# Performance work log

Hardware: AMD Instinct MI355X
Metric: run time of the kernel (lower is better)

The kernel has to match this reference:

```python
import jax, jax.numpy as jnp
import numpy as np

B, S, D = 64, 2048, 64

def setup_inputs() -> dict:
    key = jax.random.key(0)
    k1, k2, k3, k4 = jax.random.split(key, 4)
    query = jax.random.normal(k1, (B, S, D), dtype=jnp.float32)
    keyt = jax.random.normal(k2, (B, S, D), dtype=jnp.float32)
    value = jax.random.normal(k3, (B, S, D), dtype=jnp.float32)
    mask = jax.random.randint(k4, (1, S, S), 0, 2, dtype=jnp.int32)
    return {"query": query, "key": keyt, "value": value, "mask": mask}

def reference(query, key, value, mask):
    # scores: [B, S, S]
    scale = jnp.sqrt(jnp.asarray(value.shape[-1], dtype=query.dtype))
    scores = jnp.einsum('bqd,bkd->bqk', query, key) / scale
    scores = jnp.where(mask == 0, jnp.asarray(-1e9, dtype=scores.dtype), scores)
    attention_weights = jax.nn.softmax(scores, axis=-1)
    # dropout p=0.0 -> identity
    context = jnp.einsum('bqk,bkd->bqd', attention_weights, value)
    return (context, attention_weights)
```

## Files before the change

kernel.cpp:

```cpp
#include <hip/hip_runtime.h>

#define NB 64
#define NS 2048
#define ND 64
#define KSTEP 64
#define NIT (NS / KSTEP)

typedef __bf16 bf16x8 __attribute__((ext_vector_type(8)));
typedef float f32x4 __attribute__((ext_vector_type(4)));
typedef unsigned int u32;
typedef u32 u32x2 __attribute__((ext_vector_type(2)));
typedef u32 u32x4 __attribute__((ext_vector_type(4)));
typedef unsigned short u16;
typedef u16 u16x8 __attribute__((ext_vector_type(8)));

#define C2F 0.18033688011112042f

__device__ __forceinline__ float fexp2(float x) {
#if __has_builtin(__builtin_amdgcn_exp2f)
  return __builtin_amdgcn_exp2f(x);
#else
  return exp2f(x);
#endif
}
__device__ __forceinline__ float flog2(float x) {
#if __has_builtin(__builtin_amdgcn_logf)
  return __builtin_amdgcn_logf(x);
#else
  return log2f(x);
#endif
}

#define TILE_BARRIER()                                   \
  do {                                                   \
    asm volatile("s_waitcnt lgkmcnt(0)" ::: "memory");   \
    __builtin_amdgcn_s_barrier();                        \
    asm volatile("" ::: "memory");                       \
  } while (0)

__device__ __forceinline__ u16 f2bs(float x) {
  __bf16 h = (__bf16)x;
  return __builtin_bit_cast(u16, h);
}

__device__ __forceinline__ bf16x8 cvt8(f32x4 a, f32x4 b) {
  bf16x8 r;
  r[0] = (__bf16)a[0]; r[1] = (__bf16)a[1]; r[2] = (__bf16)a[2]; r[3] = (__bf16)a[3];
  r[4] = (__bf16)b[0]; r[5] = (__bf16)b[1]; r[6] = (__bf16)b[2]; r[7] = (__bf16)b[3];
  return r;
}

__global__ __launch_bounds__(256) void prep_cast_k(const float* __restrict__ K,
                                                   u16* __restrict__ Kbf) {
  const size_t i = ((size_t)blockIdx.x * 256 + threadIdx.x) * 8;
  f32x4 a = __builtin_nontemporal_load((const f32x4*)(K + i));
  f32x4 b = __builtin_nontemporal_load((const f32x4*)(K + i + 4));
  *(bf16x8*)(Kbf + i) = cvt8(a, b);
}

__global__ __launch_bounds__(256) void prep_transp_v(const float* __restrict__ V,
                                                     u16* __restrict__ VT) {
  __shared__ __attribute__((aligned(16))) u16 T[64][72];
  const int b = blockIdx.x >> 5, kt = blockIdx.x & 31;
  const float* src = V + ((size_t)b * NS + kt * 64) * ND;
  {
    const int k = threadIdx.x >> 2, d0 = (threadIdx.x & 3) * 16;
    const float* p = src + (size_t)k * ND + d0;
    f32x4 a0 = __builtin_nontemporal_load((const f32x4*)p);
    f32x4 a1 = __builtin_nontemporal_load((const f32x4*)(p + 4));
    f32x4 a2 = __builtin_nontemporal_load((const f32x4*)(p + 8));
    f32x4 a3 = __builtin_nontemporal_load((const f32x4*)(p + 12));
    *(bf16x8*)&T[k][d0]     = cvt8(a0, a1);
    *(bf16x8*)&T[k][d0 + 8] = cvt8(a2, a3);
  }
  __syncthreads();
  const int d = threadIdx.x >> 2, k0 = (threadIdx.x & 3) * 16;
  u16x8 r0, r1;
#pragma unroll
  for (int j = 0; j < 8; ++j) {
    const int P0 = k0 + j, P1 = k0 + 8 + j;
    const int s0 = 32 * (P0 >> 5) + 16 * ((P0 >> 2) & 1) + 4 * ((P0 >> 3) & 3) + (P0 & 3);
    const int s1 = 32 * (P1 >> 5) + 16 * ((P1 >> 2) & 1) + 4 * ((P1 >> 3) & 3) + (P1 & 3);
    r0[j] = T[s0][d];
    r1[j] = T[s1][d];
  }
  u16* dst = VT + ((size_t)b * ND + d) * NS + kt * 64 + k0;
  *(u16x8*)dst = r0;
  *(u16x8*)(dst + 8) = r1;
}

__global__ __launch_bounds__(256) void prep_pack_mask(const int* __restrict__ M,
                                                      unsigned long long* __restrict__ Mb) {
  const size_t i = (size_t)blockIdx.x * 256 + threadIdx.x;
  const unsigned long long bal = __ballot(M[i] != 0);
  if ((threadIdx.x & 63) == 0) Mb[i >> 6] = bal;
}

template <bool PRE>
__global__ __launch_bounds__(512, 3) void DotProductAttention_22436909154804_kernel(
    const float* __restrict__ Q, const float* __restrict__ K,
    const float* __restrict__ V, const int* __restrict__ M,
    const u16* __restrict__ Kbf, const u16* __restrict__ VTbf,
    const u32* __restrict__ Mb, float* __restrict__ ctx, float* __restrict__ wts) {
  __shared__ __attribute__((aligned(16))) u16 Kt[2][64][72];
  __shared__ __attribute__((aligned(16))) u16 Vt[2][64][72];
  __shared__ float Rs[2][64];

  const int tid  = threadIdx.x;
  const int lane = tid & 63;
  const int w    = tid >> 6;
  const int wq   = w & 3;
  const int kt   = w >> 2;
  const int g    = lane >> 4;
  const int c    = lane & 15;

  const int bid = blockIdx.x;
  const int vb  = (bid & 7) * 256 + (bid >> 3);
  const int b   = vb >> 5;
  const int qt  = vb & 31;
  const int q0w = qt * 64 + wq * 16;
  const size_t bq = (size_t)b * NS;

  const float* qp = Q + (bq + q0w + c) * ND + 8 * g;
  f32x4 qa = __builtin_nontemporal_load((const f32x4*)qp);
  f32x4 qb = __builtin_nontemporal_load((const f32x4*)(qp + 4));
  const bf16x8 qf0 = cvt8(qa, qb);
  qa = __builtin_nontemporal_load((const f32x4*)(qp + 32));
  qb = __builtin_nontemporal_load((const f32x4*)(qp + 36));
  const bf16x8 qf1 = cvt8(qa, qb);

  const u16* Kbb = PRE ? (Kbf + bq * ND) : (const u16*)nullptr;
  const u16* VTb = PRE ? (VTbf + bq * ND) : (const u16*)nullptr;
  const float* Kb32 = K + bq * ND;
  const float* Vb32 = V + bq * ND;
  const int* Mr  = M + (size_t)(q0w + c) * NS + kt * 32;
  const u32* Mbr = Mb + (size_t)(q0w + c) * (NS / 32) + kt;

  const bool isK = tid < 256;
  const int st   = tid & 255;

  auto msel = [](float e, u32 mm, int idx) -> float {
    u32 keep = (u32)(((int)(mm << (31 - idx))) >> 31);
    return __uint_as_float(__float_as_uint(e) & keep);
  };

  u16x8 sp0, sp1;
  f32x4 kf0, kf1, kf2, kf3;
  auto issueK1 = [&](int kb) {
    if (PRE) {
      const int r = tid >> 3, cc = (tid & 7) * 8;
      sp0 = *(const u16x8*)(Kbb + (size_t)(kb + r) * ND + cc);
    } else if (isK) {
      const int r = st >> 2, cc = (st & 3) * 16;
      const float* p = Kb32 + (size_t)(kb + r) * ND + cc;
      kf0 = *(const f32x4*)p;       kf1 = *(const f32x4*)(p + 4);
      kf2 = *(const f32x4*)(p + 8); kf3 = *(const f32x4*)(p + 12);
    }
  };
  auto writeK1 = [&](int buf) {
    if (PRE) {
      const int r = tid >> 3, cc = (tid & 7) * 8;
      *(u16x8*)&Kt[buf][r][cc] = sp0;
    } else if (isK) {
      const int r = st >> 2, cc = (st & 3) * 16;
      *(bf16x8*)&Kt[buf][r][cc]     = cvt8(kf0, kf1);
      *(bf16x8*)&Kt[buf][r][cc + 8] = cvt8(kf2, kf3);
    }
  };
  auto issueKV = [&](int kb) {
    if (PRE) {
      if (isK) {
        const int r = st >> 2, cc = (st & 3) * 16;
        const u16* p = Kbb + (size_t)(kb + r) * ND + cc;
        sp0 = *(const u16x8*)p; sp1 = *(const u16x8*)(p + 8);
      } else {
        const int d = st >> 2, kc = (st & 3) * 16;
        const u16* p = VTb + (size_t)d * NS + kb + kc;
        sp0 = *(const u16x8*)p; sp1 = *(const u16x8*)(p + 8);
      }
    } else {
      if (isK) {
        const int r = st >> 2, cc = (st & 3) * 16;
        const float* p = Kb32 + (size_t)(kb + r) * ND + cc;
        kf0 = *(const f32x4*)p;       kf1 = *(const f32x4*)(p + 4);
        kf2 = *(const f32x4*)(p + 8); kf3 = *(const f32x4*)(p + 12);
      } else {
        const int k = st >> 2, d0 = (st & 3) * 16;
        const float* p = Vb32 + (size_t)(kb + k) * ND + d0;
        kf0 = *(const f32x4*)p;       kf1 = *(const f32x4*)(p + 4);
        kf2 = *(const f32x4*)(p + 8); kf3 = *(const f32x4*)(p + 12);
      }
    }
  };
  auto writeKV = [&](int buf) {
    if (PRE) {
      if (isK) {
        const int r = st >> 2, cc = (st & 3) * 16;
        *(u16x8*)&Kt[buf][r][cc] = sp0; *(u16x8*)&Kt[buf][r][cc + 8] = sp1;
      } else {
        const int d = st >> 2, kc = (st & 3) * 16;
        *(u16x8*)&Vt[buf][d][kc] = sp0; *(u16x8*)&Vt[buf][d][kc + 8] = sp1;
      }
    } else {
      if (isK) {
        const int r = st >> 2, cc = (st & 3) * 16;
        *(bf16x8*)&Kt[buf][r][cc]     = cvt8(kf0, kf1);
        *(bf16x8*)&Kt[buf][r][cc + 8] = cvt8(kf2, kf3);
      } else {
        const int k = st >> 2, d0 = (st & 3) * 16;
        bf16x8 v0 = cvt8(kf0, kf1), v1 = cvt8(kf2, kf3);
#pragma unroll
        for (int j = 0; j < 8; ++j) {
          Vt[buf][d0 + j][k]     = __builtin_bit_cast(u16, v0[j]);
          Vt[buf][d0 + 8 + j][k] = __builtin_bit_cast(u16, v1[j]);
        }
      }
    }
  };

  const f32x4 zz = {0.f, 0.f, 0.f, 0.f};

  float rs = 0.f;
  issueK1(0);
  writeK1(0);
  __syncthreads();
  for (int it = 0; it < NIT; ++it) {
    const int cur = it & 1, kb = it * KSTEP;
    if (it + 1 < NIT) issueK1(kb + KSTEP);
    u32 mm = 0;
    if (PRE) mm = Mbr[kb >> 5];
#pragma unroll
    for (int j = 0; j < 2; ++j) {
      bf16x8 a0 = *(const bf16x8*)&Kt[cur][kt * 32 + 16 * j + c][8 * g];
      bf16x8 a1 = *(const bf16x8*)&Kt[cur][kt * 32 + 16 * j + c][32 + 8 * g];
      f32x4 s = __builtin_amdgcn_mfma_f32_16x16x32_bf16(a0, qf0, zz, 0, 0, 0);
      s = __builtin_amdgcn_mfma_f32_16x16x32_bf16(a1, qf1, s, 0, 0, 0);
      if (PRE) {
        rs += msel(fexp2(s[0] * C2F), mm, 16 * j + 4 * g + 0)
            + msel(fexp2(s[1] * C2F), mm, 16 * j + 4 * g + 1)
            + msel(fexp2(s[2] * C2F), mm, 16 * j + 4 * g + 2)
            + msel(fexp2(s[3] * C2F), mm, 16 * j + 4 * g + 3);
      } else {
        const int4 m4 = *(const int4*)(Mr + kb + 16 * j + 4 * g);
        rs += (m4.x ? fexp2(s[0] * C2F) : 0.f)
            + (m4.y ? fexp2(s[1] * C2F) : 0.f)
            + (m4.z ? fexp2(s[2] * C2F) : 0.f)
            + (m4.w ? fexp2(s[3] * C2F) : 0.f);
      }
    }
    if (it + 1 < NIT) writeK1((it + 1) & 1);
    TILE_BARRIER();
  }
  rs += __shfl_xor(rs, 16);
  rs += __shfl_xor(rs, 32);
  issueKV(0);
  if (lane < 16) Rs[kt][wq * 16 + c] = rs;
  __syncthreads();
  const float l2inv = -flog2(Rs[0][wq * 16 + c] + Rs[1][wq * 16 + c]);
  writeKV(0);
  __syncthreads();

  f32x4 acc[4] = {zz, zz, zz, zz};
  float* wrow = wts + (bq + q0w + c) * NS + kt * 32;
  for (int it = 0; it < NIT; ++it) {
    const int cur = it & 1, kb = it * KSTEP;
    if (it + 1 < NIT) issueKV(kb + KSTEP);
    u32 mm = 0;
    if (PRE) mm = Mbr[kb >> 5];

    u32 wpk[4];
#pragma unroll
    for (int j = 0; j < 2; ++j) {
      bf16x8 a0 = *(const bf16x8*)&Kt[cur][kt * 32 + 16 * j + c][8 * g];
      bf16x8 a1 = *(const bf16x8*)&Kt[cur][kt * 32 + 16 * j + c][32 + 8 * g];
      f32x4 s = __builtin_amdgcn_mfma_f32_16x16x32_bf16(a0, qf0, zz, 0, 0, 0);
      s = __builtin_amdgcn_mfma_f32_16x16x32_bf16(a1, qf1, s, 0, 0, 0);
      float w0, w1, w2, w3;
      if (PRE) {
        w0 = msel(fexp2(fmaf(s[0], C2F, l2inv)), mm, 16 * j + 4 * g + 0);
        w1 = msel(fexp2(fmaf(s[1], C2F, l2inv)), mm, 16 * j + 4 * g + 1);
        w2 = msel(fexp2(fmaf(s[2], C2F, l2inv)), mm, 16 * j + 4 * g + 2);
        w3 = msel(fexp2(fmaf(s[3], C2F, l2inv)), mm, 16 * j + 4 * g + 3);
      } else {
        const int4 m4 = *(const int4*)(Mr + kb + 16 * j + 4 * g);
        w0 = m4.x ? fexp2(fmaf(s[0], C2F, l2inv)) : 0.f;
        w1 = m4.y ? fexp2(fmaf(s[1], C2F, l2inv)) : 0.f;
        w2 = m4.z ? fexp2(fmaf(s[2], C2F, l2inv)) : 0.f;
        w3 = m4.w ? fexp2(fmaf(s[3], C2F, l2inv)) : 0.f;
      }
      f32x4 wv = {w0, w1, w2, w3};
      __builtin_nontemporal_store(wv, (f32x4*)(wrow + kb + 16 * j + 4 * g));
      wpk[2 * j]     = (u32)f2bs(w0) | ((u32)f2bs(w1) << 16);
      wpk[2 * j + 1] = (u32)f2bs(w2) | ((u32)f2bs(w3) << 16);
    }

    u32x4 wu = {wpk[0], wpk[1], wpk[2], wpk[3]};
    bf16x8 wb = __builtin_bit_cast(bf16x8, wu);
#pragma unroll
    for (int dt = 0; dt < 4; ++dt) {
      bf16x8 va;
      if (PRE) {
        va = *(const bf16x8*)&Vt[cur][dt * 16 + c][kt * 32 + 8 * g];
      } else {
        u32x2 vlo = *(const u32x2*)&Vt[cur][dt * 16 + c][kt * 32 + 4 * g];
        u32x2 vhi = *(const u32x2*)&Vt[cur][dt * 16 + c][kt * 32 + 16 + 4 * g];
        u32x4 vau = {vlo.x, vlo.y, vhi.x, vhi.y};
        va = __builtin_bit_cast(bf16x8, vau);
      }
      acc[dt] = __builtin_amdgcn_mfma_f32_16x16x32_bf16(va, wb, acc[dt], 0, 0, 0);
    }

    if (it + 1 < NIT) writeKV((it + 1) & 1);
    TILE_BARRIER();
  }

  float* red = (float*)&Kt[0][0][0] + wq * 1088;
  if (kt == 1) {
#pragma unroll
    for (int dt = 0; dt < 4; ++dt)
      *(f32x4*)&red[c * 68 + dt * 16 + 4 * g] = acc[dt];
  }
  __syncthreads();
  if (kt == 0) {
    float* crow = ctx + (bq + q0w + c) * ND;
#pragma unroll
    for (int dt = 0; dt < 4; ++dt) {
      f32x4 vv = acc[dt] + *(const f32x4*)&red[c * 68 + dt * 16 + 4 * g];
      __builtin_nontemporal_store(vv, (f32x4*)(crow + dt * 16 + 4 * g));
    }
  }
}

extern "C" void kernel_launch(void* const* d_in, const int* in_sizes, int n_in,
                              void* d_out, int out_size, void* d_ws, size_t ws_size,
                              hipStream_t stream) {
  const float* Q = (const float*)d_in[0];
  const float* K = (const float*)d_in[1];
  const float* V = (const float*)d_in[2];
  const int*   M = (const int*)d_in[3];
  float* ctx = (float*)d_out;
  float* wts = (float*)d_out + (size_t)NB * NS * ND;

  dim3 grid(NB * (NS / 64));
  dim3 block(512);

  constexpr size_t KBF_B = (size_t)NB * NS * ND * 2;
  constexpr size_t MB_B  = (size_t)NS * NS / 8;
  u16* Kbf = (u16*)d_ws;
  u16* VTb = (u16*)((char*)d_ws + KBF_B);
  unsigned long long* Mb64 = (unsigned long long*)((char*)d_ws + 2 * KBF_B);

  if (ws_size >= 2 * KBF_B + MB_B) {
    hipLaunchKernelGGL(prep_cast_k, dim3(NB * NS * ND / 8 / 256), dim3(256), 0, stream, K, Kbf);
    hipLaunchKernelGGL(prep_transp_v, dim3(NB * (NS / 64)), dim3(256), 0, stream, V, VTb);
    hipLaunchKernelGGL(prep_pack_mask, dim3(NS * NS / 256), dim3(256), 0, stream, M, Mb64);
    hipLaunchKernelGGL(DotProductAttention_22436909154804_kernel<true>, grid, block, 0, stream,
                       Q, K, V, M, Kbf, VTb, (const u32*)Mb64, ctx, wts);
  } else {
    hipLaunchKernelGGL(DotProductAttention_22436909154804_kernel<false>, grid, block, 0, stream,
                       Q, K, V, M, (const u16*)nullptr, (const u16*)nullptr,
                       (const u32*)nullptr, ctx, wts);
  }
}
```

Measured before the change: 346.0 us.

## Fuse prep kernels into one launch, add MFMA priority hints and packed bf16 convert

Merges the three preprocessing kernels (K cast, V transpose, mask bit-pack) into a single launch, branching on block index, to cut launch overhead and tail gaps. The mask pack switches from a wavefront ballot to per-thread int4 loads packed into 32-bit words. The main kernel wraps its MFMA sections in s_setprio hints and uses the v_cvt_pk_bf16_f32 instruction for the bf16 packing. exp2/log2 now go through the library functions rather than the raw hardware builtins, which may add range-handling instructions.

New measurement: 386.5 us. 11.7% more time.

```diff
diff --git a/kernel.cpp b/kernel.cpp
--- a/kernel.cpp
+++ b/kernel.cpp
@@ -16,20 +16,8 @@
 
 #define C2F 0.18033688011112042f
 
-__device__ __forceinline__ float fexp2(float x) {
-#if __has_builtin(__builtin_amdgcn_exp2f)
-  return __builtin_amdgcn_exp2f(x);
-#else
-  return exp2f(x);
-#endif
-}
-__device__ __forceinline__ float flog2(float x) {
-#if __has_builtin(__builtin_amdgcn_logf)
-  return __builtin_amdgcn_logf(x);
-#else
-  return log2f(x);
-#endif
-}
+__device__ __forceinline__ float fexp2(float x) { return exp2f(x); }
+__device__ __forceinline__ float flog2(float x) { return log2f(x); }
 
 #define TILE_BARRIER()                                   \
   do {                                                   \
@@ -43,6 +31,12 @@
   return __builtin_bit_cast(u16, h);
 }
 
+__device__ __forceinline__ u32 cvt_pk_bf16(float lo, float hi) {
+  u32 r;
+  asm("v_cvt_pk_bf16_f32 %0, %1, %2" : "=v"(r) : "v"(lo), "v"(hi));
+  return r;
+}
+
 __device__ __forceinline__ bf16x8 cvt8(f32x4 a, f32x4 b) {
   bf16x8 r;
   r[0] = (__bf16)a[0]; r[1] = (__bf16)a[1]; r[2] = (__bf16)a[2]; r[3] = (__bf16)a[3];
@@ -50,50 +44,61 @@
   return r;
 }
 
-__global__ __launch_bounds__(256) void prep_cast_k(const float* __restrict__ K,
-                                                   u16* __restrict__ Kbf) {
-  const size_t i = ((size_t)blockIdx.x * 256 + threadIdx.x) * 8;
-  f32x4 a = __builtin_nontemporal_load((const f32x4*)(K + i));
-  f32x4 b = __builtin_nontemporal_load((const f32x4*)(K + i + 4));
-  *(bf16x8*)(Kbf + i) = cvt8(a, b);
-}
-
-__global__ __launch_bounds__(256) void prep_transp_v(const float* __restrict__ V,
-                                                     u16* __restrict__ VT) {
+__global__ __launch_bounds__(256) void prep_fused(const float* __restrict__ K,
+                                                  const float* __restrict__ V,
+                                                  const int* __restrict__ M,
+                                                  u16* __restrict__ Kbf,
+                                                  u16* __restrict__ VT,
+                                                  u32* __restrict__ Mb) {
   __shared__ __attribute__((aligned(16))) u16 T[64][72];
-  const int b = blockIdx.x >> 5, kt = blockIdx.x & 31;
-  const float* src = V + ((size_t)b * NS + kt * 64) * ND;
-  {
-    const int k = threadIdx.x >> 2, d0 = (threadIdx.x & 3) * 16;
-    const float* p = src + (size_t)k * ND + d0;
-    f32x4 a0 = __builtin_nontemporal_load((const f32x4*)p);
-    f32x4 a1 = __builtin_nontemporal_load((const f32x4*)(p + 4));
-    f32x4 a2 = __builtin_nontemporal_load((const f32x4*)(p + 8));
-    f32x4 a3 = __builtin_nontemporal_load((const f32x4*)(p + 12));
-    *(bf16x8*)&T[k][d0]     = cvt8(a0, a1);
-    *(bf16x8*)&T[k][d0 + 8] = cvt8(a2, a3);
-  }
-  __syncthreads();
-  const int d = threadIdx.x >> 2, k0 = (threadIdx.x & 3) * 16;
-  u16x8 r0, r1;
-#pragma unroll
-  for (int j = 0; j < 8; ++j) {
-    const int P0 = k0 + j, P1 = k0 + 8 + j;
-    const int s0 = 32 * (P0 >> 5) + 16 * ((P0 >> 2) & 1) + 4 * ((P0 >> 3) & 3) + (P0 & 3);
-    const int s1 = 32 * (P1 >> 5) + 16 * ((P1 >> 2) & 1) + 4 * ((P1 >> 3) & 3) + (P1 & 3);
-    r0[j] = T[s0][d];
-    r1[j] = T[s1][d];
-  }
-  u16* dst = VT + ((size_t)b * ND + d) * NS + kt * 64 + k0;
-  *(u16x8*)dst = r0;
-  *(u16x8*)(dst + 8) = r1;
-}
-
-__global__ __launch_bounds__(256) void prep_pack_mask(const int* __restrict__ M,
-                                                      unsigned long long* __restrict__ Mb) {
-  const size_t i = (size_t)blockIdx.x * 256 + threadIdx.x;
-  const unsigned long long bal = __ballot(M[i] != 0);
-  if ((threadIdx.x & 63) == 0) Mb[i >> 6] = bal;
+  const int bid = blockIdx.x;
+  if (bid < 4096) {
+    const size_t i = ((size_t)bid * 256 + threadIdx.x) * 8;
+    f32x4 a = __builtin_nontemporal_load((const f32x4*)(K + i));
+    f32x4 b = __builtin_nontemporal_load((const f32x4*)(K + i + 4));
+    *(bf16x8*)(Kbf + i) = cvt8(a, b);
+  } else if (bid < 6144) {
+    const int vbid = bid - 4096;
+    const int b = vbid >> 5, kt = vbid & 31;
+    const float* src = V + ((size_t)b * NS + kt * 64) * ND;
+    {
+      const int k = threadIdx.x >> 2, d0 = (threadIdx.x & 3) * 16;
+      const float* p = src + (size_t)k * ND + d0;
+      f32x4 a0 = __builtin_nontemporal_load((const f32x4*)p);
+      f32x4 a1 = __builtin_nontemporal_load((const f32x4*)(p + 4));
+      f32x4 a2 = __builtin_nontemporal_load((const f32x4*)(p + 8));
+      f32x4 a3 = __builtin_nontemporal_load((const f32x4*)(p + 12));
+      *(bf16x8*)&T[k][d0]     = cvt8(a0, a1);
+      *(bf16x8*)&T[k][d0 + 8] = cvt8(a2, a3);
+    }
+    __syncthreads();
+    const int d = threadIdx.x >> 2, k0 = (threadIdx.x & 3) * 16;
+    u16x8 r0, r1;
+#pragma unroll
+    for (int j = 0; j < 8; ++j) {
+      const int P0 = k0 + j, P1 = k0 + 8 + j;
+      const int s0 = 32 * (P0 >> 5) + 16 * ((P0 >> 2) & 1) + 4 * ((P0 >> 3) & 3) + (P0 & 3);
+      const int s1 = 32 * (P1 >> 5) + 16 * ((P1 >> 2) & 1) + 4 * ((P1 >> 3) & 3) + (P1 & 3);
+      r0[j] = T[s0][d];
+      r1[j] = T[s1][d];
+    }
+    u16* dst = VT + ((size_t)b * ND + d) * NS + kt * 64 + k0;
+    *(u16x8*)dst = r0;
+    *(u16x8*)(dst + 8) = r1;
+  } else {
+    const int tg = (bid - 6144) * 256 + threadIdx.x;
+    const int4* p = (const int4*)(M + (size_t)tg * 32);
+    u32 bits = 0;
+#pragma unroll
+    for (int j = 0; j < 8; ++j) {
+      int4 m = p[j];
+      bits |= (u32)(m.x != 0) << (4 * j);
+      bits |= (u32)(m.y != 0) << (4 * j + 1);
+      bits |= (u32)(m.z != 0) << (4 * j + 2);
+      bits |= (u32)(m.w != 0) << (4 * j + 3);
+    }
+    Mb[tg] = bits;
+  }
 }
 
 template <bool PRE>
@@ -233,8 +238,10 @@
     for (int j = 0; j < 2; ++j) {
       bf16x8 a0 = *(const bf16x8*)&Kt[cur][kt * 32 + 16 * j + c][8 * g];
       bf16x8 a1 = *(const bf16x8*)&Kt[cur][kt * 32 + 16 * j + c][32 + 8 * g];
+      __builtin_amdgcn_s_setprio(1);
       f32x4 s = __builtin_amdgcn_mfma_f32_16x16x32_bf16(a0, qf0, zz, 0, 0, 0);
       s = __builtin_amdgcn_mfma_f32_16x16x32_bf16(a1, qf1, s, 0, 0, 0);
+      __builtin_amdgcn_s_setprio(0);
       if (PRE) {
         rs += msel(fexp2(s[0] * C2F), mm, 16 * j + 4 * g + 0)
             + msel(fexp2(s[1] * C2F), mm, 16 * j + 4 * g + 1)
@@ -273,8 +280,10 @@
     for (int j = 0; j < 2; ++j) {
       bf16x8 a0 = *(const bf16x8*)&Kt[cur][kt * 32 + 16 * j + c][8 * g];
       bf16x8 a1 = *(const bf16x8*)&Kt[cur][kt * 32 + 16 * j + c][32 + 8 * g];
+      __builtin_amdgcn_s_setprio(1);
       f32x4 s = __builtin_amdgcn_mfma_f32_16x16x32_bf16(a0, qf0, zz, 0, 0, 0);
       s = __builtin_amdgcn_mfma_f32_16x16x32_bf16(a1, qf1, s, 0, 0, 0);
+      __builtin_amdgcn_s_setprio(0);
       float w0, w1, w2, w3;
       if (PRE) {
         w0 = msel(fexp2(fmaf(s[0], C2F, l2inv)), mm, 16 * j + 4 * g + 0);
@@ -290,12 +299,13 @@
       }
       f32x4 wv = {w0, w1, w2, w3};
       __builtin_nontemporal_store(wv, (f32x4*)(wrow + kb + 16 * j + 4 * g));
-      wpk[2 * j]     = (u32)f2bs(w0) | ((u32)f2bs(w1) << 16);
-      wpk[2 * j + 1] = (u32)f2bs(w2) | ((u32)f2bs(w3) << 16);
+      wpk[2 * j]     = cvt_pk_bf16(w0, w1);
+      wpk[2 * j + 1] = cvt_pk_bf16(w2, w3);
     }
 
     u32x4 wu = {wpk[0], wpk[1], wpk[2], wpk[3]};
     bf16x8 wb = __builtin_bit_cast(bf16x8, wu);
+    __builtin_amdgcn_s_setprio(1);
 #pragma unroll
     for (int dt = 0; dt < 4; ++dt) {
       bf16x8 va;
@@ -309,6 +319,7 @@
       }
       acc[dt] = __builtin_amdgcn_mfma_f32_16x16x32_bf16(va, wb, acc[dt], 0, 0, 0);
     }
+    __builtin_amdgcn_s_setprio(0);
 
     if (it + 1 < NIT) writeKV((it + 1) & 1);
     TILE_BARRIER();
@@ -348,14 +359,12 @@
   constexpr size_t MB_B  = (size_t)NS * NS / 8;
   u16* Kbf = (u16*)d_ws;
   u16* VTb = (u16*)((char*)d_ws + KBF_B);
-  unsigned long long* Mb64 = (unsigned long long*)((char*)d_ws + 2 * KBF_B);
+  u32* Mb32 = (u32*)((char*)d_ws + 2 * KBF_B);
 
   if (ws_size >= 2 * KBF_B + MB_B) {
-    hipLaunchKernelGGL(prep_cast_k, dim3(NB * NS * ND / 8 / 256), dim3(256), 0, stream, K, Kbf);
-    hipLaunchKernelGGL(prep_transp_v, dim3(NB * (NS / 64)), dim3(256), 0, stream, V, VTb);
-    hipLaunchKernelGGL(prep_pack_mask, dim3(NS * NS / 256), dim3(256), 0, stream, M, Mb64);
+    hipLaunchKernelGGL(prep_fused, dim3(6656), dim3(256), 0, stream, K, V, M, Kbf, VTb, Mb32);
     hipLaunchKernelGGL(DotProductAttention_22436909154804_kernel<true>, grid, block, 0, stream,
-                       Q, K, V, M, Kbf, VTb, (const u32*)Mb64, ctx, wts);
+                       Q, K, V, M, Kbf, VTb, Mb32, ctx, wts);
   } else {
     hipLaunchKernelGGL(DotProductAttention_22436909154804_kernel<false>, grid, block, 0, stream,
                        Q, K, V, M, (const u16*)nullptr, (const u16*)nullptr,
```
